# Optimization experiments

Hardware: AMD Instinct MI355X
Metric: run time of the kernel (lower is better)

The kernel has to match this reference:

```python
import jax, jax.numpy as jnp
import numpy as np


def _conv(x, w, b):
    # x: [B,C,H,W], w: [O,I,3,3] -> SAME conv
    y = jax.lax.conv_general_dilated(x, w, window_strides=(1, 1), padding='SAME',
                                     dimension_numbers=('NCHW', 'OIHW', 'NCHW'))
    return y + b[None, :, None, None]


def _ode_f(y, W1, b1, W2, b2):
    # neural ODE vector field f(t, y) (autonomous conv net)
    return _conv(jnp.tanh(_conv(y, W1, b1)), W2, b2)


def setup_inputs() -> dict:
    key = jax.random.key(0)
    k0, k1, k2 = jax.random.split(key, 3)
    B, C, H, W, T = 16, 128, 32, 32, 25
    first_point = jax.random.normal(k0, (B, C, H, W), dtype=jnp.float32)
    # integration grid over [0, 0.96], one RK4 step per interval (torchdiffeq 'rk4')
    time_steps_to_predict = jnp.arange(T, dtype=jnp.float32) * 0.04
    W1 = jax.random.normal(k1, (C, C, 3, 3), dtype=jnp.float32) * 0.05
    b1 = jnp.zeros((C,), dtype=jnp.float32)
    W2 = jax.random.normal(k2, (C, C, 3, 3), dtype=jnp.float32) * 0.05
    b2 = jnp.zeros((C,), dtype=jnp.float32)
    return {'first_point': first_point, 'time_steps_to_predict': time_steps_to_predict,
            'W1': W1, 'b1': b1, 'W2': W2, 'b2': b2}


def reference(first_point, time_steps_to_predict, W1, b1, W2, b2):
    # DiffeqSolver.forward (nru=nru2=False): pred = odeint(f, y0, t) with fixed-grid RK4
    # (one step per consecutive time pair), then permute [T,B,C,H,W] -> [B,T,C,H,W].
    f = lambda y: _ode_f(y, W1, b1, W2, b2)

    def rk4_step(y, dt):
        k1 = f(y)
        k2 = f(y + 0.5 * dt * k1)
        k3 = f(y + 0.5 * dt * k2)
        k4 = f(y + dt * k3)
        y1 = y + (dt / 6.0) * (k1 + 2.0 * k2 + 2.0 * k3 + k4)
        return y1, y1

    dts = jnp.diff(time_steps_to_predict)           # [T-1]
    _, ys = jax.lax.scan(rk4_step, first_point, dts)  # [T-1,B,C,H,W]
    pred = jnp.concatenate([first_point[None], ys], axis=0)  # [T,B,C,H,W]
    return jnp.transpose(pred, (1, 0, 2, 3, 4))     # [B,T,C,H,W]
```

## Files before the change

kernel.cpp:

```cpp
#include <hip/hip_runtime.h>
#include <hip/hip_bf16.h>
#include <math.h>

typedef __attribute__((ext_vector_type(8))) short bf16x8;
typedef __attribute__((ext_vector_type(4))) float f32x4;
typedef __attribute__((ext_vector_type(4))) unsigned short u16x4;

#define B_   16
#define C_   128
#define CHW_ 131072
#define STR_ 138

__device__ __forceinline__ unsigned short f2bf(float f) {
  union { float f; unsigned int i; } v; v.f = f;
  unsigned int lsb = (v.i >> 16) & 1u;
  v.i += 0x7fffu + lsb;
  return (unsigned short)(v.i >> 16);
}

__device__ __forceinline__ float fast_tanh(float x) {
  float e = __expf(2.f * x);
  return 1.f - 2.f * __builtin_amdgcn_rcpf(e + 1.f);
}

__global__ void prep_weights(const float* __restrict__ W1, const float* __restrict__ W2,
                             unsigned short* __restrict__ w1bf, unsigned short* __restrict__ w2bf) {
  int j = blockIdx.x * 256 + threadIdx.x;
  if (j >= 2 * 147456) return;
  int which = j / 147456;
  int r = j - which * 147456;
  int ks = r >> 12;
  int co = (r >> 5) & 127;
  int c5 = r & 31;
  int off = ks >> 2;
  int ci  = (ks & 3) * 32 + c5;
  const float* src = which ? W2 : W1;
  unsigned short* dst = which ? w2bf : w1bf;
  dst[r] = f2bf(src[(co * 128 + ci) * 9 + off]);
}

__global__ void init_copy(const float* __restrict__ y0, float* __restrict__ y32,
                          float* __restrict__ dout) {
  int i = blockIdx.x * 256 + threadIdx.x;
  if (i >= B_ * CHW_) return;
  float v = y0[i];
  y32[i] = v;
  int b = i >> 17, chw = i & (CHW_ - 1);
  dout[b * 25 * CHW_ + chw] = v;
}

__global__ void init_transpose(const float* __restrict__ y0, unsigned short* __restrict__ tmp_bf) {
  __shared__ float t[32][33];
  int blk = blockIdx.x;
  int b = blk >> 7;
  int rem = blk & 127;
  int co0 = (rem >> 5) * 32;
  int p0  = (rem & 31) * 32;
  int tx = threadIdx.x & 31, ty = threadIdx.x >> 5;
  #pragma unroll
  for (int k = 0; k < 4; k++) {
    int cl = ty + k * 8;
    t[cl][tx] = y0[b * CHW_ + (co0 + cl) * 1024 + p0 + tx];
  }
  __syncthreads();
  #pragma unroll
  for (int k = 0; k < 4; k++) {
    int pl = ty + k * 8;
    tmp_bf[(b * 1024 + p0 + pl) * 128 + co0 + tx] = f2bf(t[tx][pl]);
  }
}

template<int ST>
__global__ __launch_bounds__(512, 1)
void fused_stage(const unsigned short* __restrict__ w1bf,
                 const unsigned short* __restrict__ w2bf,
                 const float* __restrict__ b1v, const float* __restrict__ b2v,
                 unsigned short* __restrict__ tmp_bf,
                 float* __restrict__ y32, float* __restrict__ acc32,
                 float* __restrict__ dout, const float* __restrict__ tarr, int step)
{
  __shared__ unsigned short IT[204 * STR_];
  __shared__ unsigned short ZT[136 * STR_];
  const int tid  = threadIdx.x;
  const int img  = blockIdx.x >> 4;
  const int r0   = (blockIdx.x & 15) * 2;
  const int lane = tid & 63;
  const int wave = tid >> 6;
  const int lhi  = lane >> 4;
  const int llo  = lane & 15;

  const unsigned short* a1base = w1bf + (wave * 16 + llo) * 32 + lhi * 8;
  const unsigned short* a2base = w2bf + (wave * 16 + llo) * 32 + lhi * 8;

  float t0 = tarr[step];
  float t1 = tarr[step + 1];
  asm volatile("" : "+v"(t1));
  const float dt = t1 - t0;
  const float dt6 = dt * (1.f / 6.f), dt3 = dt * (1.f / 3.f), dth = dt * 0.5f;

  for (int chunk = tid; chunk < 204 * 16 + 128; chunk += 512) {
    if (chunk < 204 * 16) {
      int pix = chunk >> 4;
      int oct = chunk & 15;
      int ir = pix / 34, ic = pix - ir * 34;
      int gr = r0 - 2 + ir, gc = ic - 1;
      bf16x8 v = {0, 0, 0, 0, 0, 0, 0, 0};
      if ((unsigned)gr < 32u && (unsigned)gc < 32u)
        v = *(const bf16x8*)(tmp_bf + ((img * 32 + gr) * 32 + gc) * 128 + oct * 8);
      *(bf16x8*)(IT + pix * STR_ + oct * 8) = v;
    } else {
      int padidx = chunk - 204 * 16;
      int zp  = padidx >> 4;
      int oct = padidx & 15;
      int zpix = (zp >> 1) * 34 + ((zp & 1) ? 33 : 0);
      bf16x8 z = {0, 0, 0, 0, 0, 0, 0, 0};
      *(bf16x8*)(ZT + zpix * STR_ + oct * 8) = z;
    }
  }
  __syncthreads();

  {
    const int co = wave * 16 + lhi * 4;
    f32x4 bia = *(const f32x4*)(b1v + co);
    f32x4 a1[4][2];
    #pragma unroll
    for (int i = 0; i < 4; i++) { a1[i][0] = (f32x4){0,0,0,0}; a1[i][1] = (f32x4){0,0,0,0}; }
    #pragma unroll
    for (int dw = 0; dw < 3; ++dw) {
      #pragma unroll
      for (int kk = 0; kk < 4; ++kk) {
        bf16x8 bfr[6][2];
        #pragma unroll
        for (int rr = 0; rr < 6; ++rr) {
          const int prow = rr * 34 + llo + dw;
          bfr[rr][0] = *(const bf16x8*)(IT + prow * STR_ + kk * 32 + lhi * 8);
          bfr[rr][1] = *(const bf16x8*)(IT + (prow + 16) * STR_ + kk * 32 + lhi * 8);
        }
        bf16x8 afr[3];
        #pragma unroll
        for (int dh = 0; dh < 3; ++dh)
          afr[dh] = *(const bf16x8*)(a1base + ((dh * 3 + dw) * 4 + kk) * 4096);
        #pragma unroll
        for (int dh = 0; dh < 3; ++dh)
          #pragma unroll
          for (int zr = 0; zr < 4; ++zr)
            #pragma unroll
            for (int spt = 0; spt < 2; ++spt)
              a1[zr][spt] = __builtin_amdgcn_mfma_f32_16x16x32_bf16(afr[dh], bfr[zr + dh][spt], a1[zr][spt], 0, 0, 0);
      }
    }
    #pragma unroll
    for (int zr = 0; zr < 4; ++zr) {
      const bool live = (unsigned)(r0 - 1 + zr) < 32u;
      #pragma unroll
      for (int spt = 0; spt < 2; ++spt) {
        const int c = spt * 16 + llo;
        u16x4 pk;
        #pragma unroll
        for (int reg = 0; reg < 4; ++reg)
          pk[reg] = live ? f2bf(fast_tanh(a1[zr][spt][reg] + bia[reg])) : (unsigned short)0;
        *(u16x4*)(ZT + (zr * 34 + c + 1) * STR_ + co) = pk;
      }
    }
  }
  __syncthreads();

  {
    const int co0 = wave * 16 + lhi * 4;
    f32x4 bia = *(const f32x4*)(b2v + co0);
    float ypre[2][2][4], apre[2][2][4];
    #pragma unroll
    for (int q = 0; q < 2; ++q)
      #pragma unroll
      for (int spt = 0; spt < 2; ++spt) {
        const int idx0 = img * CHW_ + co0 * 1024 + (r0 + q) * 32 + spt * 16 + llo;
        #pragma unroll
        for (int reg = 0; reg < 4; ++reg) {
          if constexpr (ST <= 3) ypre[q][spt][reg] = y32[idx0 + reg * 1024];
          if constexpr (ST >= 2) apre[q][spt][reg] = acc32[idx0 + reg * 1024];
        }
      }

    f32x4 a2[2][2];
    #pragma unroll
    for (int i = 0; i < 2; i++) { a2[i][0] = (f32x4){0,0,0,0}; a2[i][1] = (f32x4){0,0,0,0}; }
    #pragma unroll
    for (int dw = 0; dw < 3; ++dw) {
      #pragma unroll
      for (int kk = 0; kk < 4; ++kk) {
        bf16x8 bfr[4][2];
        #pragma unroll
        for (int rr = 0; rr < 4; ++rr) {
          const int zpix = rr * 34 + llo + dw;
          bfr[rr][0] = *(const bf16x8*)(ZT + zpix * STR_ + kk * 32 + lhi * 8);
          bfr[rr][1] = *(const bf16x8*)(ZT + (zpix + 16) * STR_ + kk * 32 + lhi * 8);
        }
        bf16x8 afr[3];
        #pragma unroll
        for (int dh = 0; dh < 3; ++dh)
          afr[dh] = *(const bf16x8*)(a2base + ((dh * 3 + dw) * 4 + kk) * 4096);
        #pragma unroll
        for (int dh = 0; dh < 3; ++dh)
          #pragma unroll
          for (int q = 0; q < 2; ++q)
            #pragma unroll
            for (int spt = 0; spt < 2; ++spt)
              a2[q][spt] = __builtin_amdgcn_mfma_f32_16x16x32_bf16(afr[dh], bfr[q + dh][spt], a2[q][spt], 0, 0, 0);
      }
    }

    #pragma unroll
    for (int q = 0; q < 2; ++q) {
      const int row = r0 + q;
      #pragma unroll
      for (int spt = 0; spt < 2; ++spt) {
        const int col = spt * 16 + llo;
        const int pnhwc = (img * 1024 + row * 32 + col) * 128 + co0;
        const int idx0  = img * CHW_ + co0 * 1024 + row * 32 + col;
        u16x4 pk;
        #pragma unroll
        for (int reg = 0; reg < 4; ++reg) {
          float kv = a2[q][spt][reg] + bia[reg];
          int id = idx0 + reg * 1024;
          float tv;
          if constexpr (ST == 1)      { float yv = ypre[q][spt][reg]; acc32[id] = yv + dt6 * kv; tv = yv + dth * kv; }
          else if constexpr (ST == 2) { float yv = ypre[q][spt][reg]; acc32[id] = apre[q][spt][reg] + dt3 * kv; tv = yv + dth * kv; }
          else if constexpr (ST == 3) { float yv = ypre[q][spt][reg]; acc32[id] = apre[q][spt][reg] + dt3 * kv; tv = yv + dt * kv; }
          else {
            tv = apre[q][spt][reg] + dt6 * kv;
            y32[id] = tv;
            dout[(img * 25 + step + 1) * CHW_ + co0 * 1024 + row * 32 + col + reg * 1024] = tv;
          }
          pk[reg] = f2bf(tv);
        }
        *(u16x4*)(tmp_bf + pnhwc) = pk;
      }
    }
  }
}

extern "C" void kernel_launch(void* const* d_in, const int* in_sizes, int n_in,
                              void* d_out, int out_size, void* d_ws, size_t ws_size,
                              hipStream_t stream) {
  const float* y0   = (const float*)d_in[0];
  const float* tarr = (const float*)d_in[1];
  const float* W1   = (const float*)d_in[2];
  const float* b1   = (const float*)d_in[3];
  const float* W2   = (const float*)d_in[4];
  const float* b2   = (const float*)d_in[5];
  float* dout = (float*)d_out;

  char* ws = (char*)d_ws;
  float* y32             = (float*)(ws);
  float* acc32           = (float*)(ws + (8u << 20));
  unsigned short* tmp_bf = (unsigned short*)(ws + (16u << 20));
  unsigned short* w1bf   = (unsigned short*)(ws + (20u << 20));
  unsigned short* w2bf   = (unsigned short*)(ws + (20u << 20) + 294912);

  prep_weights<<<(2 * 147456 + 255) / 256, 256, 0, stream>>>(W1, W2, w1bf, w2bf);
  init_copy<<<(B_ * CHW_ + 255) / 256, 256, 0, stream>>>(y0, y32, dout);
  init_transpose<<<2048, 256, 0, stream>>>(y0, tmp_bf);

  for (int step = 0; step < 24; ++step) {
    fused_stage<1><<<256, 512, 0, stream>>>(w1bf, w2bf, b1, b2, tmp_bf, y32, acc32, dout, tarr, step);
    fused_stage<2><<<256, 512, 0, stream>>>(w1bf, w2bf, b1, b2, tmp_bf, y32, acc32, dout, tarr, step);
    fused_stage<3><<<256, 512, 0, stream>>>(w1bf, w2bf, b1, b2, tmp_bf, y32, acc32, dout, tarr, step);
    fused_stage<4><<<256, 512, 0, stream>>>(w1bf, w2bf, b1, b2, tmp_bf, y32, acc32, dout, tarr, step);
  }
}
```

Baseline: 2.247 ms.

## Store activations with zero halo and feed conv1 operands directly from global memory

The bf16 NHWC activation buffer gets a one-pixel zero-padded halo, so the first convolution can load its B fragments straight from global/L2 memory. This removes the LDS staging tile and its barrier. Loop order changes so each spatial half loads its fragments once per kk, and launch bounds are raised to allow more occupancy. In exchange, each operand read goes to cache or global memory instead of LDS, and reads that overlap between waves are no longer shared.

```diff
diff --git a/kernel.cpp b/kernel.cpp
--- a/kernel.cpp
+++ b/kernel.cpp
@@ -10,6 +10,7 @@
 #define C_   128
 #define CHW_ 131072
 #define STR_ 138
+#define TH_  34
 
 __device__ __forceinline__ unsigned short f2bf(float f) {
   union { float f; unsigned int i; } v; v.f = f;
@@ -49,7 +50,7 @@
   dout[b * 25 * CHW_ + chw] = v;
 }
 
-__global__ void init_transpose(const float* __restrict__ y0, unsigned short* __restrict__ tmp_bf) {
+__global__ void init_transpose(const float* __restrict__ y0, unsigned short* __restrict__ tmpH) {
   __shared__ float t[32][33];
   int blk = blockIdx.x;
   int b = blk >> 7;
@@ -66,20 +67,21 @@
   #pragma unroll
   for (int k = 0; k < 4; k++) {
     int pl = ty + k * 8;
-    tmp_bf[(b * 1024 + p0 + pl) * 128 + co0 + tx] = f2bf(t[tx][pl]);
+    int p = p0 + pl;
+    int row = p >> 5, col = p & 31;
+    tmpH[((b * TH_ + row + 1) * TH_ + col + 1) * 128 + co0 + tx] = f2bf(t[tx][pl]);
   }
 }
 
 template<int ST>
-__global__ __launch_bounds__(512, 1)
+__global__ __launch_bounds__(512, 4)
 void fused_stage(const unsigned short* __restrict__ w1bf,
                  const unsigned short* __restrict__ w2bf,
                  const float* __restrict__ b1v, const float* __restrict__ b2v,
-                 unsigned short* __restrict__ tmp_bf,
+                 unsigned short* __restrict__ tmpH,
                  float* __restrict__ y32, float* __restrict__ acc32,
                  float* __restrict__ dout, const float* __restrict__ tarr, int step)
 {
-  __shared__ unsigned short IT[204 * STR_];
   __shared__ unsigned short ZT[136 * STR_];
   const int tid  = threadIdx.x;
   const int img  = blockIdx.x >> 4;
@@ -91,6 +93,7 @@
 
   const unsigned short* a1base = w1bf + (wave * 16 + llo) * 32 + lhi * 8;
   const unsigned short* a2base = w2bf + (wave * 16 + llo) * 32 + lhi * 8;
+  const unsigned short* bbase = tmpH + (((long)img * TH_ + (r0 - 1)) * TH_ + llo) * 128 + lhi * 8;
 
   float t0 = tarr[step];
   float t1 = tarr[step + 1];
@@ -98,26 +101,13 @@
   const float dt = t1 - t0;
   const float dt6 = dt * (1.f / 6.f), dt3 = dt * (1.f / 3.f), dth = dt * 0.5f;
 
-  for (int chunk = tid; chunk < 204 * 16 + 128; chunk += 512) {
-    if (chunk < 204 * 16) {
-      int pix = chunk >> 4;
-      int oct = chunk & 15;
-      int ir = pix / 34, ic = pix - ir * 34;
-      int gr = r0 - 2 + ir, gc = ic - 1;
-      bf16x8 v = {0, 0, 0, 0, 0, 0, 0, 0};
-      if ((unsigned)gr < 32u && (unsigned)gc < 32u)
-        v = *(const bf16x8*)(tmp_bf + ((img * 32 + gr) * 32 + gc) * 128 + oct * 8);
-      *(bf16x8*)(IT + pix * STR_ + oct * 8) = v;
-    } else {
-      int padidx = chunk - 204 * 16;
-      int zp  = padidx >> 4;
-      int oct = padidx & 15;
-      int zpix = (zp >> 1) * 34 + ((zp & 1) ? 33 : 0);
-      bf16x8 z = {0, 0, 0, 0, 0, 0, 0, 0};
-      *(bf16x8*)(ZT + zpix * STR_ + oct * 8) = z;
-    }
-  }
-  __syncthreads();
+  if (tid < 128) {
+    int zp  = tid >> 4;
+    int oct = tid & 15;
+    int zpix = (zp >> 1) * 34 + ((zp & 1) ? 33 : 0);
+    bf16x8 z = {0, 0, 0, 0, 0, 0, 0, 0};
+    *(bf16x8*)(ZT + zpix * STR_ + oct * 8) = z;
+  }
 
   {
     const int co = wave * 16 + lhi * 4;
@@ -129,24 +119,22 @@
     for (int dw = 0; dw < 3; ++dw) {
       #pragma unroll
       for (int kk = 0; kk < 4; ++kk) {
-        bf16x8 bfr[6][2];
-        #pragma unroll
-        for (int rr = 0; rr < 6; ++rr) {
-          const int prow = rr * 34 + llo + dw;
-          bfr[rr][0] = *(const bf16x8*)(IT + prow * STR_ + kk * 32 + lhi * 8);
-          bfr[rr][1] = *(const bf16x8*)(IT + (prow + 16) * STR_ + kk * 32 + lhi * 8);
-        }
         bf16x8 afr[3];
         #pragma unroll
         for (int dh = 0; dh < 3; ++dh)
           afr[dh] = *(const bf16x8*)(a1base + ((dh * 3 + dw) * 4 + kk) * 4096);
         #pragma unroll
-        for (int dh = 0; dh < 3; ++dh)
-          #pragma unroll
-          for (int zr = 0; zr < 4; ++zr)
+        for (int spt = 0; spt < 2; ++spt) {
+          bf16x8 bfr[6];
+          #pragma unroll
+          for (int rr = 0; rr < 6; ++rr)
+            bfr[rr] = *(const bf16x8*)(bbase + ((long)rr * TH_ + spt * 16 + dw) * 128 + kk * 32);
+          #pragma unroll
+          for (int dh = 0; dh < 3; ++dh)
             #pragma unroll
-            for (int spt = 0; spt < 2; ++spt)
-              a1[zr][spt] = __builtin_amdgcn_mfma_f32_16x16x32_bf16(afr[dh], bfr[zr + dh][spt], a1[zr][spt], 0, 0, 0);
+            for (int zr = 0; zr < 4; ++zr)
+              a1[zr][spt] = __builtin_amdgcn_mfma_f32_16x16x32_bf16(afr[dh], bfr[zr + dh], a1[zr][spt], 0, 0, 0);
+        }
       }
     }
     #pragma unroll
@@ -188,24 +176,22 @@
     for (int dw = 0; dw < 3; ++dw) {
       #pragma unroll
       for (int kk = 0; kk < 4; ++kk) {
-        bf16x8 bfr[4][2];
-        #pragma unroll
-        for (int rr = 0; rr < 4; ++rr) {
-          const int zpix = rr * 34 + llo + dw;
-          bfr[rr][0] = *(const bf16x8*)(ZT + zpix * STR_ + kk * 32 + lhi * 8);
-          bfr[rr][1] = *(const bf16x8*)(ZT + (zpix + 16) * STR_ + kk * 32 + lhi * 8);
-        }
         bf16x8 afr[3];
         #pragma unroll
         for (int dh = 0; dh < 3; ++dh)
           afr[dh] = *(const bf16x8*)(a2base + ((dh * 3 + dw) * 4 + kk) * 4096);
         #pragma unroll
-        for (int dh = 0; dh < 3; ++dh)
-          #pragma unroll
-          for (int q = 0; q < 2; ++q)
+        for (int spt = 0; spt < 2; ++spt) {
+          bf16x8 bfr[4];
+          #pragma unroll
+          for (int rr = 0; rr < 4; ++rr)
+            bfr[rr] = *(const bf16x8*)(ZT + (rr * 34 + spt * 16 + llo + dw) * STR_ + kk * 32 + lhi * 8);
+          #pragma unroll
+          for (int dh = 0; dh < 3; ++dh)
             #pragma unroll
-            for (int spt = 0; spt < 2; ++spt)
-              a2[q][spt] = __builtin_amdgcn_mfma_f32_16x16x32_bf16(afr[dh], bfr[q + dh][spt], a2[q][spt], 0, 0, 0);
+            for (int q = 0; q < 2; ++q)
+              a2[q][spt] = __builtin_amdgcn_mfma_f32_16x16x32_bf16(afr[dh], bfr[q + dh], a2[q][spt], 0, 0, 0);
+        }
       }
     }
 
@@ -215,7 +201,7 @@
       #pragma unroll
       for (int spt = 0; spt < 2; ++spt) {
         const int col = spt * 16 + llo;
-        const int pnhwc = (img * 1024 + row * 32 + col) * 128 + co0;
+        const int phalo = (((long)img * TH_ + row + 1) * TH_ + col + 1) * 128 + co0;
         const int idx0  = img * CHW_ + co0 * 1024 + row * 32 + col;
         u16x4 pk;
         #pragma unroll
@@ -233,7 +219,7 @@
           }
           pk[reg] = f2bf(tv);
         }
-        *(u16x4*)(tmp_bf + pnhwc) = pk;
+        *(u16x4*)(tmpH + phalo) = pk;
       }
     }
   }
@@ -251,20 +237,23 @@
   float* dout = (float*)d_out;
 
   char* ws = (char*)d_ws;
-  float* y32             = (float*)(ws);
-  float* acc32           = (float*)(ws + (8u << 20));
-  unsigned short* tmp_bf = (unsigned short*)(ws + (16u << 20));
-  unsigned short* w1bf   = (unsigned short*)(ws + (20u << 20));
-  unsigned short* w2bf   = (unsigned short*)(ws + (20u << 20) + 294912);
+  float* y32           = (float*)(ws);
+  float* acc32         = (float*)(ws + (8u << 20));
+  unsigned short* tmpH = (unsigned short*)(ws + (16u << 20));
+  unsigned short* w1bf = (unsigned short*)(ws + (22u << 20));
+  unsigned short* w2bf = (unsigned short*)(ws + (22u << 20) + 294912);
+
+  const size_t tmpH_bytes = (size_t)B_ * TH_ * TH_ * 128 * 2;
 
   prep_weights<<<(2 * 147456 + 255) / 256, 256, 0, stream>>>(W1, W2, w1bf, w2bf);
   init_copy<<<(B_ * CHW_ + 255) / 256, 256, 0, stream>>>(y0, y32, dout);
-  init_transpose<<<2048, 256, 0, stream>>>(y0, tmp_bf);
+  hipMemsetAsync(tmpH, 0, tmpH_bytes, stream);
+  init_transpose<<<2048, 256, 0, stream>>>(y0, tmpH);
 
   for (int step = 0; step < 24; ++step) {
-    fused_stage<1><<<256, 512, 0, stream>>>(w1bf, w2bf, b1, b2, tmp_bf, y32, acc32, dout, tarr, step);
-    fused_stage<2><<<256, 512, 0, stream>>>(w1bf, w2bf, b1, b2, tmp_bf, y32, acc32, dout, tarr, step);
-    fused_stage<3><<<256, 512, 0, stream>>>(w1bf, w2bf, b1, b2, tmp_bf, y32, acc32, dout, tarr, step);
-    fused_stage<4><<<256, 512, 0, stream>>>(w1bf, w2bf, b1, b2, tmp_bf, y32, acc32, dout, tarr, step);
-  }
-}
+    fused_stage<1><<<256, 512, 0, stream>>>(w1bf, w2bf, b1, b2, tmpH, y32, acc32, dout, tarr, step);
+    fused_stage<2><<<256, 512, 0, stream>>>(w1bf, w2bf, b1, b2, tmpH, y32, acc32, dout, tarr, step);
+    fused_stage<3><<<256, 512, 0, stream>>>(w1bf, w2bf, b1, b2, tmpH, y32, acc32, dout, tarr, step);
+    fused_stage<4><<<256, 512, 0, stream>>>(w1bf, w2bf, b1, b2, tmpH, y32, acc32, dout, tarr, step);
+  }
+}
```

After: 4.714 ms. 110% more time.

## Specialize waves: half compute conv1 with doubled channel tiles, half prefetch state

Applied to the files above, without the earlier changes.

Conv1 is now computed by only waves 0-3, each handling 32 output channels (two 16-channel tiles) so every B-fragment LDS read feeds twice as many MFMAs. Waves 4-7 instead issue the global loads of the y/acc state for the second stage while conv1 runs, and waves 0-3 issue theirs after the barrier. This cuts LDS traffic for conv1 and overlaps global state loads with compute. In exchange, half the waves sit idle during conv1 and the conv1 waves hold more accumulator registers.

```diff
diff --git a/kernel.cpp b/kernel.cpp
--- a/kernel.cpp
+++ b/kernel.cpp
@@ -89,7 +89,6 @@
   const int lhi  = lane >> 4;
   const int llo  = lane & 15;
 
-  const unsigned short* a1base = w1bf + (wave * 16 + llo) * 32 + lhi * 8;
   const unsigned short* a2base = w2bf + (wave * 16 + llo) * 32 + lhi * 8;
 
   float t0 = tarr[step];
@@ -119,12 +118,38 @@
   }
   __syncthreads();
 
-  {
-    const int co = wave * 16 + lhi * 4;
-    f32x4 bia = *(const f32x4*)(b1v + co);
-    f32x4 a1[4][2];
-    #pragma unroll
-    for (int i = 0; i < 4; i++) { a1[i][0] = (f32x4){0,0,0,0}; a1[i][1] = (f32x4){0,0,0,0}; }
+  const int co0 = wave * 16 + lhi * 4;
+  float ypre[2][2][4], apre[2][2][4];
+  auto prefetch_state = [&]() {
+    #pragma unroll
+    for (int q = 0; q < 2; ++q)
+      #pragma unroll
+      for (int spt = 0; spt < 2; ++spt) {
+        const int idx0 = img * CHW_ + co0 * 1024 + (r0 + q) * 32 + spt * 16 + llo;
+        #pragma unroll
+        for (int reg = 0; reg < 4; ++reg) {
+          if constexpr (ST <= 3) ypre[q][spt][reg] = y32[idx0 + reg * 1024];
+          if constexpr (ST >= 2) apre[q][spt][reg] = acc32[idx0 + reg * 1024];
+        }
+      }
+  };
+
+  if (wave >= 4) {
+    prefetch_state();
+  } else {
+    const int cob = wave * 32;
+    const unsigned short* a1b = w1bf + (cob + llo) * 32 + lhi * 8;
+    f32x4 bia[2];
+    bia[0] = *(const f32x4*)(b1v + cob + lhi * 4);
+    bia[1] = *(const f32x4*)(b1v + cob + 16 + lhi * 4);
+    f32x4 a1[2][4][2];
+    #pragma unroll
+    for (int i = 0; i < 2; i++)
+      #pragma unroll
+      for (int j = 0; j < 4; j++) {
+        a1[i][j][0] = (f32x4){0, 0, 0, 0};
+        a1[i][j][1] = (f32x4){0, 0, 0, 0};
+      }
     #pragma unroll
     for (int dw = 0; dw < 3; ++dw) {
       #pragma unroll
@@ -136,51 +161,48 @@
           bfr[rr][0] = *(const bf16x8*)(IT + prow * STR_ + kk * 32 + lhi * 8);
           bfr[rr][1] = *(const bf16x8*)(IT + (prow + 16) * STR_ + kk * 32 + lhi * 8);
         }
-        bf16x8 afr[3];
-        #pragma unroll
-        for (int dh = 0; dh < 3; ++dh)
-          afr[dh] = *(const bf16x8*)(a1base + ((dh * 3 + dw) * 4 + kk) * 4096);
+        bf16x8 afr[2][3];
+        #pragma unroll
+        for (int dh = 0; dh < 3; ++dh) {
+          const int ksoff = ((dh * 3 + dw) * 4 + kk) * 4096;
+          afr[0][dh] = *(const bf16x8*)(a1b + ksoff);
+          afr[1][dh] = *(const bf16x8*)(a1b + ksoff + 512);
+        }
         #pragma unroll
         for (int dh = 0; dh < 3; ++dh)
           #pragma unroll
-          for (int zr = 0; zr < 4; ++zr)
+          for (int ct = 0; ct < 2; ++ct)
             #pragma unroll
-            for (int spt = 0; spt < 2; ++spt)
-              a1[zr][spt] = __builtin_amdgcn_mfma_f32_16x16x32_bf16(afr[dh], bfr[zr + dh][spt], a1[zr][spt], 0, 0, 0);
-      }
-    }
-    #pragma unroll
-    for (int zr = 0; zr < 4; ++zr) {
-      const bool live = (unsigned)(r0 - 1 + zr) < 32u;
-      #pragma unroll
-      for (int spt = 0; spt < 2; ++spt) {
-        const int c = spt * 16 + llo;
-        u16x4 pk;
-        #pragma unroll
-        for (int reg = 0; reg < 4; ++reg)
-          pk[reg] = live ? f2bf(fast_tanh(a1[zr][spt][reg] + bia[reg])) : (unsigned short)0;
-        *(u16x4*)(ZT + (zr * 34 + c + 1) * STR_ + co) = pk;
+            for (int zr = 0; zr < 4; ++zr)
+              #pragma unroll
+              for (int spt = 0; spt < 2; ++spt)
+                a1[ct][zr][spt] = __builtin_amdgcn_mfma_f32_16x16x32_bf16(afr[ct][dh], bfr[zr + dh][spt], a1[ct][zr][spt], 0, 0, 0);
+      }
+    }
+    #pragma unroll
+    for (int ct = 0; ct < 2; ++ct) {
+      const int co = cob + ct * 16 + lhi * 4;
+      #pragma unroll
+      for (int zr = 0; zr < 4; ++zr) {
+        const bool live = (unsigned)(r0 - 1 + zr) < 32u;
+        #pragma unroll
+        for (int spt = 0; spt < 2; ++spt) {
+          const int c = spt * 16 + llo;
+          u16x4 pk;
+          #pragma unroll
+          for (int reg = 0; reg < 4; ++reg)
+            pk[reg] = live ? f2bf(fast_tanh(a1[ct][zr][spt][reg] + bia[ct][reg])) : (unsigned short)0;
+          *(u16x4*)(ZT + (zr * 34 + c + 1) * STR_ + co) = pk;
+        }
       }
     }
   }
   __syncthreads();
 
+  if (wave < 4) prefetch_state();
+
   {
-    const int co0 = wave * 16 + lhi * 4;
     f32x4 bia = *(const f32x4*)(b2v + co0);
-    float ypre[2][2][4], apre[2][2][4];
-    #pragma unroll
-    for (int q = 0; q < 2; ++q)
-      #pragma unroll
-      for (int spt = 0; spt < 2; ++spt) {
-        const int idx0 = img * CHW_ + co0 * 1024 + (r0 + q) * 32 + spt * 16 + llo;
-        #pragma unroll
-        for (int reg = 0; reg < 4; ++reg) {
-          if constexpr (ST <= 3) ypre[q][spt][reg] = y32[idx0 + reg * 1024];
-          if constexpr (ST >= 2) apre[q][spt][reg] = acc32[idx0 + reg * 1024];
-        }
-      }
-
     f32x4 a2[2][2];
     #pragma unroll
     for (int i = 0; i < 2; i++) { a2[i][0] = (f32x4){0,0,0,0}; a2[i][1] = (f32x4){0,0,0,0}; }
```

Result: slower. 2.301 ms (+2.4%).

## Switch conv MFMA tiles from 16x16x32 to 32x32x16 with new wave partition

Applied to the files above, without the earlier changes.

Replaces the 16x16x32 bf16 MFMA tiling with 32x32x16 MFMAs. The weight prep layout becomes a K-slice of 16, and the eight waves are split into four output-channel groups of 32 times two row groups. Each wave now loads fewer LDS B fragments per MFMA, which raises compute per LDS read. The cost is a different register footprint and epilogue mapping, with per-lane stores now strided by channel.

```diff
diff --git a/kernel.cpp b/kernel.cpp
--- a/kernel.cpp
+++ b/kernel.cpp
@@ -4,6 +4,7 @@
 
 typedef __attribute__((ext_vector_type(8))) short bf16x8;
 typedef __attribute__((ext_vector_type(4))) float f32x4;
+typedef __attribute__((ext_vector_type(16))) float f32x16;
 typedef __attribute__((ext_vector_type(4))) unsigned short u16x4;
 
 #define B_   16
@@ -29,11 +30,11 @@
   if (j >= 2 * 147456) return;
   int which = j / 147456;
   int r = j - which * 147456;
-  int ks = r >> 12;
-  int co = (r >> 5) & 127;
-  int c5 = r & 31;
-  int off = ks >> 2;
-  int ci  = (ks & 3) * 32 + c5;
+  int s  = r >> 11;
+  int co = (r >> 4) & 127;
+  int kl = r & 15;
+  int off = s >> 3;
+  int ci  = (s & 7) * 16 + kl;
   const float* src = which ? W2 : W1;
   unsigned short* dst = which ? w2bf : w1bf;
   dst[r] = f2bf(src[(co * 128 + ci) * 9 + off]);
@@ -86,11 +87,16 @@
   const int r0   = (blockIdx.x & 15) * 2;
   const int lane = tid & 63;
   const int wave = tid >> 6;
-  const int lhi  = lane >> 4;
-  const int llo  = lane & 15;
-
-  const unsigned short* a1base = w1bf + (wave * 16 + llo) * 32 + lhi * 8;
-  const unsigned short* a2base = w2bf + (wave * 16 + llo) * 32 + lhi * 8;
+  const int ln31 = lane & 31;
+  const int lk   = (lane >> 5) * 8;
+  const int lm4  = (lane >> 5) * 4;
+
+  const int cob = (wave & 3) * 32;
+  const int zrp = (wave >> 2) * 2;
+  const int rw  = wave >> 2;
+
+  const unsigned short* a1base = w1bf + (cob + ln31) * 16 + lk;
+  const unsigned short* a2base = w2bf + (cob + ln31) * 16 + lk;
 
   float t0 = tarr[step];
   float t1 = tarr[step + 1];
@@ -120,121 +126,111 @@
   __syncthreads();
 
   {
-    const int co = wave * 16 + lhi * 4;
-    f32x4 bia = *(const f32x4*)(b1v + co);
-    f32x4 a1[4][2];
-    #pragma unroll
-    for (int i = 0; i < 4; i++) { a1[i][0] = (f32x4){0,0,0,0}; a1[i][1] = (f32x4){0,0,0,0}; }
+    f32x16 acc1[2];
+    #pragma unroll
+    for (int q = 0; q < 2; ++q)
+      #pragma unroll
+      for (int i = 0; i < 16; ++i) acc1[q][i] = 0.f;
+
     #pragma unroll
     for (int dw = 0; dw < 3; ++dw) {
       #pragma unroll
-      for (int kk = 0; kk < 4; ++kk) {
-        bf16x8 bfr[6][2];
-        #pragma unroll
-        for (int rr = 0; rr < 6; ++rr) {
-          const int prow = rr * 34 + llo + dw;
-          bfr[rr][0] = *(const bf16x8*)(IT + prow * STR_ + kk * 32 + lhi * 8);
-          bfr[rr][1] = *(const bf16x8*)(IT + (prow + 16) * STR_ + kk * 32 + lhi * 8);
+      for (int t = 0; t < 8; ++t) {
+        bf16x8 bfr[4];
+        #pragma unroll
+        for (int rr = 0; rr < 4; ++rr) {
+          const int px = (zrp + rr) * 34 + ln31 + dw;
+          bfr[rr] = *(const bf16x8*)(IT + px * STR_ + t * 16 + lk);
         }
         bf16x8 afr[3];
         #pragma unroll
         for (int dh = 0; dh < 3; ++dh)
-          afr[dh] = *(const bf16x8*)(a1base + ((dh * 3 + dw) * 4 + kk) * 4096);
+          afr[dh] = *(const bf16x8*)(a1base + ((dh * 3 + dw) * 8 + t) * 2048);
         #pragma unroll
         for (int dh = 0; dh < 3; ++dh)
           #pragma unroll
-          for (int zr = 0; zr < 4; ++zr)
-            #pragma unroll
-            for (int spt = 0; spt < 2; ++spt)
-              a1[zr][spt] = __builtin_amdgcn_mfma_f32_16x16x32_bf16(afr[dh], bfr[zr + dh][spt], a1[zr][spt], 0, 0, 0);
-      }
-    }
-    #pragma unroll
-    for (int zr = 0; zr < 4; ++zr) {
+          for (int q = 0; q < 2; ++q)
+            acc1[q] = __builtin_amdgcn_mfma_f32_32x32x16_bf16(afr[dh], bfr[q + dh], acc1[q], 0, 0, 0);
+      }
+    }
+    #pragma unroll
+    for (int q = 0; q < 2; ++q) {
+      const int zr = zrp + q;
       const bool live = (unsigned)(r0 - 1 + zr) < 32u;
       #pragma unroll
-      for (int spt = 0; spt < 2; ++spt) {
-        const int c = spt * 16 + llo;
+      for (int g = 0; g < 4; ++g) {
+        const int cog = cob + 8 * g + lm4;
+        f32x4 bia = *(const f32x4*)(b1v + cog);
         u16x4 pk;
         #pragma unroll
-        for (int reg = 0; reg < 4; ++reg)
-          pk[reg] = live ? f2bf(fast_tanh(a1[zr][spt][reg] + bia[reg])) : (unsigned short)0;
-        *(u16x4*)(ZT + (zr * 34 + c + 1) * STR_ + co) = pk;
+        for (int i = 0; i < 4; ++i)
+          pk[i] = live ? f2bf(fast_tanh(acc1[q][4 * g + i] + bia[i])) : (unsigned short)0;
+        *(u16x4*)(ZT + (zr * 34 + ln31 + 1) * STR_ + cog) = pk;
       }
     }
   }
   __syncthreads();
 
   {
-    const int co0 = wave * 16 + lhi * 4;
-    f32x4 bia = *(const f32x4*)(b2v + co0);
-    float ypre[2][2][4], apre[2][2][4];
-    #pragma unroll
-    for (int q = 0; q < 2; ++q)
-      #pragma unroll
-      for (int spt = 0; spt < 2; ++spt) {
-        const int idx0 = img * CHW_ + co0 * 1024 + (r0 + q) * 32 + spt * 16 + llo;
-        #pragma unroll
-        for (int reg = 0; reg < 4; ++reg) {
-          if constexpr (ST <= 3) ypre[q][spt][reg] = y32[idx0 + reg * 1024];
-          if constexpr (ST >= 2) apre[q][spt][reg] = acc32[idx0 + reg * 1024];
-        }
-      }
-
-    f32x4 a2[2][2];
-    #pragma unroll
-    for (int i = 0; i < 2; i++) { a2[i][0] = (f32x4){0,0,0,0}; a2[i][1] = (f32x4){0,0,0,0}; }
+    const int row = r0 + rw;
+    float ypre[16], apre[16];
+    #pragma unroll
+    for (int g = 0; g < 4; ++g) {
+      const int cog = cob + 8 * g + lm4;
+      #pragma unroll
+      for (int i = 0; i < 4; ++i) {
+        const int id = img * CHW_ + (cog + i) * 1024 + row * 32 + ln31;
+        if constexpr (ST <= 3) ypre[4 * g + i] = y32[id];
+        if constexpr (ST >= 2) apre[4 * g + i] = acc32[id];
+      }
+    }
+
+    f32x16 a2;
+    #pragma unroll
+    for (int i = 0; i < 16; ++i) a2[i] = 0.f;
     #pragma unroll
     for (int dw = 0; dw < 3; ++dw) {
       #pragma unroll
-      for (int kk = 0; kk < 4; ++kk) {
-        bf16x8 bfr[4][2];
-        #pragma unroll
-        for (int rr = 0; rr < 4; ++rr) {
-          const int zpix = rr * 34 + llo + dw;
-          bfr[rr][0] = *(const bf16x8*)(ZT + zpix * STR_ + kk * 32 + lhi * 8);
-          bfr[rr][1] = *(const bf16x8*)(ZT + (zpix + 16) * STR_ + kk * 32 + lhi * 8);
+      for (int t = 0; t < 8; ++t) {
+        bf16x8 bfr[3];
+        #pragma unroll
+        for (int dh = 0; dh < 3; ++dh) {
+          const int px = (rw + dh) * 34 + ln31 + dw;
+          bfr[dh] = *(const bf16x8*)(ZT + px * STR_ + t * 16 + lk);
         }
         bf16x8 afr[3];
         #pragma unroll
         for (int dh = 0; dh < 3; ++dh)
-          afr[dh] = *(const bf16x8*)(a2base + ((dh * 3 + dw) * 4 + kk) * 4096);
-        #pragma unroll
-        for (int dh = 0; dh < 3; ++dh)
-          #pragma unroll
-          for (int q = 0; q < 2; ++q)
-            #pragma unroll
-            for (int spt = 0; spt < 2; ++spt)
-              a2[q][spt] = __builtin_amdgcn_mfma_f32_16x16x32_bf16(afr[dh], bfr[q + dh][spt], a2[q][spt], 0, 0, 0);
-      }
-    }
-
-    #pragma unroll
-    for (int q = 0; q < 2; ++q) {
-      const int row = r0 + q;
-      #pragma unroll
-      for (int spt = 0; spt < 2; ++spt) {
-        const int col = spt * 16 + llo;
-        const int pnhwc = (img * 1024 + row * 32 + col) * 128 + co0;
-        const int idx0  = img * CHW_ + co0 * 1024 + row * 32 + col;
-        u16x4 pk;
-        #pragma unroll
-        for (int reg = 0; reg < 4; ++reg) {
-          float kv = a2[q][spt][reg] + bia[reg];
-          int id = idx0 + reg * 1024;
-          float tv;
-          if constexpr (ST == 1)      { float yv = ypre[q][spt][reg]; acc32[id] = yv + dt6 * kv; tv = yv + dth * kv; }
-          else if constexpr (ST == 2) { float yv = ypre[q][spt][reg]; acc32[id] = apre[q][spt][reg] + dt3 * kv; tv = yv + dth * kv; }
-          else if constexpr (ST == 3) { float yv = ypre[q][spt][reg]; acc32[id] = apre[q][spt][reg] + dt3 * kv; tv = yv + dt * kv; }
-          else {
-            tv = apre[q][spt][reg] + dt6 * kv;
-            y32[id] = tv;
-            dout[(img * 25 + step + 1) * CHW_ + co0 * 1024 + row * 32 + col + reg * 1024] = tv;
-          }
-          pk[reg] = f2bf(tv);
+          afr[dh] = *(const bf16x8*)(a2base + ((dh * 3 + dw) * 8 + t) * 2048);
+        #pragma unroll
+        for (int dh = 0; dh < 3; ++dh)
+          a2 = __builtin_amdgcn_mfma_f32_32x32x16_bf16(afr[dh], bfr[dh], a2, 0, 0, 0);
+      }
+    }
+
+    #pragma unroll
+    for (int g = 0; g < 4; ++g) {
+      const int cog = cob + 8 * g + lm4;
+      f32x4 bia = *(const f32x4*)(b2v + cog);
+      const int pnhwc = (img * 1024 + row * 32 + ln31) * 128 + cog;
+      u16x4 pk;
+      #pragma unroll
+      for (int i = 0; i < 4; ++i) {
+        const int e = 4 * g + i;
+        float kv = a2[e] + bia[i];
+        const int id = img * CHW_ + (cog + i) * 1024 + row * 32 + ln31;
+        float tv;
+        if constexpr (ST == 1)      { float yv = ypre[e]; acc32[id] = yv + dt6 * kv; tv = yv + dth * kv; }
+        else if constexpr (ST == 2) { float yv = ypre[e]; acc32[id] = apre[e] + dt3 * kv; tv = yv + dth * kv; }
+        else if constexpr (ST == 3) { float yv = ypre[e]; acc32[id] = apre[e] + dt3 * kv; tv = yv + dt * kv; }
+        else {
+          tv = apre[e] + dt6 * kv;
+          y32[id] = tv;
+          dout[(img * 25 + step + 1) * CHW_ + (cog + i) * 1024 + row * 32 + ln31] = tv;
         }
-        *(u16x4*)(tmp_bf + pnhwc) = pk;
-      }
+        pk[i] = f2bf(tv);
+      }
+      *(u16x4*)(tmp_bf + pnhwc) = pk;
     }
   }
 }
```

Measured after the change: 2.392 ms. 6.4% more time.
